# Optimization experiments

Measured on AMD Instinct MI355X. Metric: run time of the kernel, lower is better.

The kernel has to match this reference:

```python
import jax, jax.numpy as jnp
import numpy as np

B, IN_DIM, L = 8, 1, 512
D_MODEL, N_LAYERS, D_STATE, HORIZON, D_CONV, EXPAND = 512, 4, 16, 96, 4, 2
D_INNER = EXPAND * D_MODEL            # 1024
DT_RANK = (D_MODEL + 15) // 16        # ceil(d_model/16) = 32
EPS = 1e-5


def setup_inputs() -> dict:
    key = jax.random.key(0)
    ks = jax.random.split(key, 10)
    s = 0.02
    f32 = jnp.float32
    return {
        "x": jax.random.normal(ks[0], (B, IN_DIM, L), f32),
        "embed_w": jax.random.normal(ks[1], (D_MODEL, IN_DIM), f32) * s,
        "embed_b": jnp.zeros((D_MODEL,), f32),
        "norm_w": jnp.ones((N_LAYERS, D_MODEL), f32),
        "in_proj_w": jax.random.normal(ks[2], (N_LAYERS, 2 * D_INNER, D_MODEL), f32) * s,
        "conv_w": jax.random.normal(ks[3], (N_LAYERS, D_INNER, D_CONV), f32) * s,
        "conv_b": jnp.zeros((N_LAYERS, D_INNER), f32),
        "x_proj_w": jax.random.normal(ks[4], (N_LAYERS, DT_RANK + 2 * D_STATE, D_INNER), f32) * s,
        "dt_w": jax.random.normal(ks[5], (N_LAYERS, D_INNER, DT_RANK), f32) * s,
        "dt_b": jax.random.uniform(ks[6], (N_LAYERS, D_INNER), f32, -4.0, -2.0),
        "A_log": jnp.log(jnp.broadcast_to(jnp.arange(1, D_STATE + 1, dtype=f32), (N_LAYERS, D_INNER, D_STATE))),
        "D": jnp.ones((N_LAYERS, D_INNER), f32),
        "out_proj_w": jax.random.normal(ks[7], (N_LAYERS, D_MODEL, D_INNER), f32) * s,
        "head_w": jax.random.normal(ks[8], (HORIZON, D_MODEL), f32) * s,
        "head_b": jnp.zeros((HORIZON,), f32),
    }


def _rmsnorm(x, w):
    return x * jax.lax.rsqrt(jnp.mean(x * x, axis=-1, keepdims=True) + EPS) * w


def _mamba_layer(x, norm_w, in_w, conv_w, conv_b, xproj_w, dt_w, dt_b, A_log, Dp, out_w):
    res = x
    h = _rmsnorm(x, norm_w)
    xz = h @ in_w.T                       # (B, L, 2*I)
    xin, z = jnp.split(xz, 2, axis=-1)
    # causal depthwise conv1d over L (left-pad d_conv-1)
    lhs = jnp.swapaxes(xin, 1, 2)         # (B, I, L)
    rhs = conv_w[:, None, :]              # (I, 1, K)
    conv = jax.lax.conv_general_dilated(
        lhs, rhs, (1,), [(D_CONV - 1, 0)],
        dimension_numbers=("NCH", "OIH", "NCH"), feature_group_count=D_INNER)
    xin = jax.nn.silu(jnp.swapaxes(conv, 1, 2) + conv_b)   # (B, L, I)
    dbc = xin @ xproj_w.T                                   # (B, L, dt_rank+2N)
    delta = jax.nn.softplus(dbc[..., :DT_RANK] @ dt_w.T + dt_b)  # (B, L, I)
    Bc = dbc[..., DT_RANK:DT_RANK + D_STATE]                # (B, L, N)
    Cc = dbc[..., DT_RANK + D_STATE:]                       # (B, L, N)
    A = -jnp.exp(A_log)                                     # (I, N)
    dA = jnp.exp(delta[..., None] * A)                      # (B, L, I, N)
    dBx = delta[..., None] * Bc[:, :, None, :] * xin[..., None]

    def step(hst, inputs):
        a, bx = inputs
        hst = a * hst + bx
        return hst, hst

    h0 = jnp.zeros((x.shape[0], D_INNER, D_STATE), x.dtype)
    _, hs = jax.lax.scan(step, h0, (jnp.swapaxes(dA, 0, 1), jnp.swapaxes(dBx, 0, 1)))
    hs = jnp.swapaxes(hs, 0, 1)                             # (B, L, I, N)
    y = jnp.einsum("blin,bln->bli", hs, Cc) + Dp * xin
    y = y * jax.nn.silu(z)
    return res + y @ out_w.T


def reference(x, embed_w, embed_b, norm_w, in_proj_w, conv_w, conv_b, x_proj_w,
              dt_w, dt_b, A_log, D, out_proj_w, head_w, head_b):
    h = jnp.swapaxes(x, 1, 2) @ embed_w.T + embed_b         # (B, L, d_model)
    for i in range(N_LAYERS):
        h = _mamba_layer(h, norm_w[i], in_proj_w[i], conv_w[i], conv_b[i],
                         x_proj_w[i], dt_w[i], dt_b[i], A_log[i], D[i], out_proj_w[i])
    return h[:, -1, :] @ head_w.T + head_b                  # (B, horizon)
```

## Files before the change

kernel.cpp:

```cpp
#include <hip/hip_runtime.h>
#include <hip/hip_bf16.h>

#define B_  8
#define L_  512
#define DM  512
#define NL  4
#define DS  16
#define HOR 96
#define DC  4
#define DI  1024
#define DTR 32

#define CHUNK 16
#define NCHK (L_/CHUNK)

typedef __bf16 bf16_t;
typedef __bf16 b8_t __attribute__((ext_vector_type(8)));
typedef float  f4_t __attribute__((ext_vector_type(4)));

#define LOG2E 1.44269504088896f

__device__ __forceinline__ float sigmoidf_(float x){ return 1.f/(1.f+__expf(-x)); }

__device__ __forceinline__ void async16(const bf16_t* g, bf16_t* l){
  __builtin_amdgcn_global_load_lds((const __attribute__((address_space(1))) void*)g,
                                   (__attribute__((address_space(3))) void*)l, 16, 0, 0);
}

__global__ __launch_bounds__(256) void k_prep(const float* __restrict__ p0, bf16_t* __restrict__ o0,
                                              const float* __restrict__ p1, bf16_t* __restrict__ o1,
                                              const float* __restrict__ p2, bf16_t* __restrict__ o2,
                                              const float* __restrict__ p3, bf16_t* __restrict__ o3,
                                              const float* __restrict__ x, const float* __restrict__ ew,
                                              const float* __restrict__ eb, float* __restrict__ h){
  int blk = blockIdx.x;
  if (blk < 6528){
    int j = blk*256 + threadIdx.x;
    const int S0=1048576, S1=65536, S2=32768;
    const float* src; bf16_t* dst;
    if (j < S0){ src=p0; dst=o0; }
    else if ((j-=S0) < S1){ src=p1; dst=o1; }
    else if ((j-=S1) < S2){ src=p2; dst=o2; }
    else { j-=S2; src=p3; dst=o3; }
    f4_t v = ((const f4_t*)src)[j];
    bf16_t* o = dst + (size_t)j*4;
    o[0]=(bf16_t)v[0]; o[1]=(bf16_t)v[1]; o[2]=(bf16_t)v[2]; o[3]=(bf16_t)v[3];
  } else {
    int j = (blk-6528)*256 + threadIdx.x;
    int idx = j*4;
    int d = idx & (DM-1); int t = idx >> 9;
    float xv = x[t];
    f4_t w = *(const f4_t*)(ew + d);
    f4_t b = *(const f4_t*)(eb + d);
    f4_t v;
    #pragma unroll
    for (int c=0;c<4;c++) v[c] = xv*w[c] + b[c];
    *(f4_t*)(h + idx) = v;
  }
}

__global__ __launch_bounds__(256) void k_rms(const float* __restrict__ h, const float* __restrict__ w,
                                             bf16_t* __restrict__ o){
  int t = blockIdx.x; int tid = threadIdx.x;
  const float* hp = h + (size_t)t*DM;
  float v0 = hp[tid], v1 = hp[tid+256];
  float s = v0*v0 + v1*v1;
  #pragma unroll
  for (int m=32;m;m>>=1) s += __shfl_xor(s, m);
  __shared__ float red[4];
  if ((tid&63)==0) red[tid>>6]=s;
  __syncthreads();
  float tot = red[0]+red[1]+red[2]+red[3];
  float sc = rsqrtf(tot*(1.f/DM) + 1e-5f);
  o[(size_t)t*DM + tid]       = (bf16_t)(v0*sc*w[tid]);
  o[(size_t)t*DM + tid + 256] = (bf16_t)(v1*sc*w[tid+256]);
}

__global__ __launch_bounds__(256) void k_g128(const bf16_t* __restrict__ A, int lda,
                                              const bf16_t* __restrict__ W, int ldw,
                                              int K, bf16_t* __restrict__ Cbf, int ldc){
  __shared__ bf16_t As[4*128*32];
  __shared__ bf16_t Ws[4*128*32];
  int tid = threadIdx.x;
  int m0 = blockIdx.y*128, n0 = blockIdx.x*128;
  int wave = tid>>6, lane = tid&63;
  int wm = (wave>>1)*64, wn = (wave&1)*64;
  int lr = lane&15, q = lane>>4;
  int rs = tid>>2, cs = (tid&3)*8;
  f4_t acc[4][4] = {};
  for (int k0=0;k0<K;k0+=128){
    #pragma unroll
    for (int p=0;p<4;p++){
      #pragma unroll
      for (int s=0;s<2;s++){
        int row = s*64 + rs;
        async16(A + (size_t)(m0+row)*lda + k0 + p*32 + cs, As + p*4096 + s*2048 + tid*8);
        async16(W + (size_t)(n0+row)*ldw + k0 + p*32 + cs, Ws + p*4096 + s*2048 + tid*8);
      }
    }
    __syncthreads();
    #pragma unroll
    for (int p=0;p<4;p++){
      b8_t a[4], b[4];
      #pragma unroll
      for (int i=0;i<4;i++) a[i] = *(const b8_t*)(As + p*4096 + (wm+i*16+lr)*32 + q*8);
      #pragma unroll
      for (int j=0;j<4;j++) b[j] = *(const b8_t*)(Ws + p*4096 + (wn+j*16+lr)*32 + q*8);
      #pragma unroll
      for (int i=0;i<4;i++)
        #pragma unroll
        for (int j=0;j<4;j++)
          acc[i][j] = __builtin_amdgcn_mfma_f32_16x16x32_bf16(a[i], b[j], acc[i][j], 0,0,0);
    }
    __syncthreads();
  }
  #pragma unroll
  for (int i=0;i<4;i++)
  #pragma unroll
  for (int j=0;j<4;j++){
    int col = n0 + wn + j*16 + lr;
    int rb  = m0 + wm + i*16 + q*4;
    #pragma unroll
    for (int r=0;r<4;r++)
      Cbf[(size_t)(rb+r)*ldc + col] = (bf16_t)acc[i][j][r];
  }
}

__global__ __launch_bounds__(256) void k_gout64(const bf16_t* __restrict__ A,
                                                const bf16_t* __restrict__ W,
                                                float* __restrict__ C){
  __shared__ bf16_t As[8*64*32];
  __shared__ bf16_t Ws[8*64*32];
  int tid = threadIdx.x;
  int m0 = blockIdx.y*64, n0 = blockIdx.x*64;
  int wave = tid>>6, lane = tid&63;
  int wm = (wave>>1)*32, wn = (wave&1)*32;
  int lr = lane&15, q = lane>>4;
  int e0 = tid*8, r0 = e0>>5, c0 = e0&31;
  f4_t acc[2][2] = {};
  for (int k0=0;k0<DI;k0+=256){
    #pragma unroll
    for (int p=0;p<8;p++){
      async16(A + (size_t)(m0+r0)*DI + k0 + p*32 + c0, As + p*2048 + e0);
      async16(W + (size_t)(n0+r0)*DI + k0 + p*32 + c0, Ws + p*2048 + e0);
    }
    __syncthreads();
    #pragma unroll
    for (int p=0;p<8;p++){
      b8_t a[2], b[2];
      #pragma unroll
      for (int i=0;i<2;i++) a[i] = *(const b8_t*)(As + p*2048 + (wm+i*16+lr)*32 + q*8);
      #pragma unroll
      for (int j=0;j<2;j++) b[j] = *(const b8_t*)(Ws + p*2048 + (wn+j*16+lr)*32 + q*8);
      #pragma unroll
      for (int i=0;i<2;i++)
        #pragma unroll
        for (int j=0;j<2;j++)
          acc[i][j] = __builtin_amdgcn_mfma_f32_16x16x32_bf16(a[i], b[j], acc[i][j], 0,0,0);
    }
    __syncthreads();
  }
  #pragma unroll
  for (int i=0;i<2;i++)
  #pragma unroll
  for (int j=0;j<2;j++){
    int col = n0 + wn + j*16 + lr;
    int rb  = m0 + wm + i*16 + q*4;
    #pragma unroll
    for (int r=0;r<4;r++){
      size_t off = (size_t)(rb+r)*DM + col;
      C[off] = C[off] + acc[i][j][r];
    }
  }
}

__global__ __launch_bounds__(256) void k_dbc(const bf16_t* __restrict__ xzbf, const float* __restrict__ cw,
                                             const float* __restrict__ cb, const bf16_t* __restrict__ wxp,
                                             float* __restrict__ part, bf16_t* __restrict__ xinbf){
  __shared__ bf16_t As[4*64*32];
  __shared__ bf16_t Ws[4*64*32];
  int tid = threadIdx.x;
  int m0 = blockIdx.x*64;
  int z = blockIdx.y;
  int kbase = z*128;
  int wave = tid>>6, lane = tid&63;
  int wm = (wave>>1)*32, wn = (wave&1)*32;
  int lr = lane&15, q = lane>>4;
  int e0 = tid*8, r0 = e0>>5, c0 = e0&31;
  int gt = m0 + r0;
  int l  = gt & (L_-1);
  f4_t acc[2][2] = {};
  #pragma unroll
  for (int p=0;p<4;p++){
    int ch = kbase + p*32 + c0;
    float cv[8];
    #pragma unroll
    for (int c=0;c<8;c++) cv[c] = cb[ch+c];
    #pragma unroll
    for (int k=0;k<DC;k++){
      if (l + k - (DC-1) >= 0){
        b8_t xv = *(const b8_t*)(xzbf + (size_t)(gt + k - (DC-1))*(2*DI) + ch);
        #pragma unroll
        for (int c=0;c<8;c++) cv[c] += (float)xv[c] * cw[(ch+c)*DC + k];
      }
    }
    b8_t av;
    #pragma unroll
    for (int c=0;c<8;c++){ float s = cv[c]*sigmoidf_(cv[c]); av[c] = (bf16_t)s; }
    *(b8_t*)(As + p*2048 + e0) = av;
    *(b8_t*)(xinbf + (size_t)gt*DI + ch) = av;
    async16(wxp + (size_t)r0*DI + kbase + p*32 + c0, Ws + p*2048 + e0);
  }
  __syncthreads();
  #pragma unroll
  for (int p=0;p<4;p++){
    b8_t a[2], b[2];
    #pragma unroll
    for (int i=0;i<2;i++) a[i] = *(const b8_t*)(As + p*2048 + (wm+i*16+lr)*32 + q*8);
    #pragma unroll
    for (int j=0;j<2;j++) b[j] = *(const b8_t*)(Ws + p*2048 + (wn+j*16+lr)*32 + q*8);
    #pragma unroll
    for (int i=0;i<2;i++)
      #pragma unroll
      for (int j=0;j<2;j++)
        acc[i][j] = __builtin_amdgcn_mfma_f32_16x16x32_bf16(a[i], b[j], acc[i][j], 0,0,0);
  }
  float* P = part + (size_t)z*(B_*L_*64);
  #pragma unroll
  for (int i=0;i<2;i++)
  #pragma unroll
  for (int j=0;j<2;j++){
    int col = wn + j*16 + lr;
    int rb  = m0 + wm + i*16 + q*4;
    #pragma unroll
    for (int r=0;r<4;r++) P[(size_t)(rb+r)*64 + col] = acc[i][j][r];
  }
}

__global__ __launch_bounds__(256) void k_dt(const float* __restrict__ part, const bf16_t* __restrict__ wdt,
                                            const float* __restrict__ dtb, float* __restrict__ dbc,
                                            bf16_t* __restrict__ delta){
  __shared__ bf16_t As[64*32];
  __shared__ bf16_t Ws[64*32];
  int tid = threadIdx.x;
  int m0 = blockIdx.y*64, n0 = blockIdx.x*64;
  const size_t S = (size_t)B_*L_*64;
  int r0 = tid>>2, c0 = (tid&3)*8;
  int gt = m0 + r0;
  size_t base = (size_t)gt*64 + c0;
  f4_t s0 = *(const f4_t*)(part + base);
  f4_t s1 = *(const f4_t*)(part + base + 4);
  #pragma unroll
  for (int z=1;z<8;z++){
    s0 += *(const f4_t*)(part + z*S + base);
    s1 += *(const f4_t*)(part + z*S + base + 4);
  }
  b8_t av;
  #pragma unroll
  for (int c=0;c<4;c++){ av[c] = (bf16_t)s0[c]; av[4+c] = (bf16_t)s1[c]; }
  *(b8_t*)(As + tid*8) = av;
  if (n0 == 0){
    f4_t t0 = *(const f4_t*)(part + base + 32);
    f4_t t1 = *(const f4_t*)(part + base + 36);
    #pragma unroll
    for (int z=1;z<8;z++){
      t0 += *(const f4_t*)(part + z*S + base + 32);
      t1 += *(const f4_t*)(part + z*S + base + 36);
    }
    *(f4_t*)(dbc + base + 32) = t0;
    *(f4_t*)(dbc + base + 36) = t1;
  }
  async16(wdt + (size_t)(n0+r0)*DTR + c0, Ws + tid*8);
  __syncthreads();
  int wave = tid>>6, lane = tid&63;
  int wm = (wave>>1)*32, wn = (wave&1)*32;
  int lr = lane&15, q = lane>>4;
  b8_t a[2], b[2];
  #pragma unroll
  for (int i=0;i<2;i++) a[i] = *(const b8_t*)(As + (wm+i*16+lr)*32 + q*8);
  #pragma unroll
  for (int j=0;j<2;j++) b[j] = *(const b8_t*)(Ws + (wn+j*16+lr)*32 + q*8);
  f4_t acc[2][2] = {};
  #pragma unroll
  for (int i=0;i<2;i++)
    #pragma unroll
    for (int j=0;j<2;j++)
      acc[i][j] = __builtin_amdgcn_mfma_f32_16x16x32_bf16(a[i], b[j], acc[i][j], 0,0,0);
  #pragma unroll
  for (int i=0;i<2;i++)
  #pragma unroll
  for (int j=0;j<2;j++){
    int col = n0 + wn + j*16 + lr;
    int rb  = m0 + wm + i*16 + q*4;
    #pragma unroll
    for (int r=0;r<4;r++){
      float xv = acc[i][j][r] + dtb[col];
      float v = (xv>20.f)?xv:log1pf(__expf(xv));
      delta[(size_t)(rb+r)*DI + col] = (bf16_t)v;
    }
  }
}

__global__ __launch_bounds__(256) void k_scan_p1(const bf16_t* __restrict__ delta, const bf16_t* __restrict__ xin,
                                                 const float* __restrict__ dbc, const float* __restrict__ Alog,
                                                 bf16_t* __restrict__ hend, bf16_t* __restrict__ aprod){
  __shared__ bf16_t des[CHUNK][256];
  __shared__ bf16_t xs[CHUNK][256];
  __shared__ float Bs[CHUNK][DS];
  int tid = threadIdx.x;
  int blk = blockIdx.x;
  int chgrp = blk & 3;
  int chunk = (blk>>2) & (NCHK-1);
  int b = blk >> 7;
  int ch0 = chgrp<<8;
  int ch = ch0 + tid;
  int t0 = (b<<9) + chunk*CHUNK;
  #pragma unroll
  for (int idx=tid; idx<CHUNK*32; idx+=256){
    int row = idx>>5, c = (idx&31)*8;
    *(b8_t*)(&des[row][c]) = *(const b8_t*)(delta + (size_t)(t0+row)*DI + ch0 + c);
    *(b8_t*)(&xs[row][c])  = *(const b8_t*)(xin   + (size_t)(t0+row)*DI + ch0 + c);
  }
  {
    int ll = tid>>4, n = tid&15;
    Bs[ll][n] = dbc[(t0+ll)*64 + DTR + n];
  }
  __syncthreads();
  float An2[DS], h[DS];
  const f4_t* Ap = (const f4_t*)(Alog + ch*DS);
  #pragma unroll
  for (int v=0;v<4;v++){
    f4_t a4 = Ap[v];
    #pragma unroll
    for (int k=0;k<4;k++){ An2[v*4+k] = -__expf(a4[k])*LOG2E; h[v*4+k]=0.f; }
  }
  float sde = 0.f;
  #pragma unroll
  for (int l=0;l<CHUNK;l++){
    float de = (float)des[l][tid];
    float xv = (float)xs[l][tid];
    float dx = de*xv;
    sde += de;
    #pragma unroll
    for (int n=0;n<DS;n++){
      float dA = exp2f(de*An2[n]);
      h[n] = dA*h[n] + dx*Bs[l][n];
    }
  }
  size_t base = ((size_t)chunk*(B_*DI) + (b<<10) + ch)*DS;
  b8_t hv[2], av[2];
  #pragma unroll
  for (int v=0;v<2;v++)
    #pragma unroll
    for (int k=0;k<8;k++){
      hv[v][k] = (bf16_t)h[v*8+k];
      av[v][k] = (bf16_t)exp2f(An2[v*8+k]*sde);
    }
  ((b8_t*)(hend + base))[0] = hv[0]; ((b8_t*)(hend + base))[1] = hv[1];
  ((b8_t*)(aprod + base))[0] = av[0]; ((b8_t*)(aprod + base))[1] = av[1];
}

__global__ __launch_bounds__(256) void k_scan_p2(const bf16_t* __restrict__ hend, bf16_t* __restrict__ ap_hin){
  int g = blockIdx.x*256 + threadIdx.x;
  float h = 0.f;
  for (int c=0;c<NCHK;c++){
    size_t off = (size_t)c*(B_*DI*DS) + g;
    float a = (float)ap_hin[off];
    float e = (float)hend[off];
    ap_hin[off] = (bf16_t)h;
    h = a*h + e;
  }
}

__global__ __launch_bounds__(256) void k_scan_p3(const bf16_t* __restrict__ delta, const bf16_t* __restrict__ xz,
                                                 const bf16_t* __restrict__ xin,
                                                 const float* __restrict__ dbc, const float* __restrict__ Alog,
                                                 const bf16_t* __restrict__ hin, const float* __restrict__ Dp,
                                                 bf16_t* __restrict__ ybf){
  __shared__ bf16_t des[CHUNK][256];
  __shared__ bf16_t xs[CHUNK][256];
  __shared__ bf16_t zs[CHUNK][256];
  __shared__ float Bs[CHUNK][DS];
  __shared__ float Cs[CHUNK][DS];
  int tid = threadIdx.x;
  int blk = blockIdx.x;
  int chgrp = blk & 3;
  int chunk = (blk>>2) & (NCHK-1);
  int b = blk >> 7;
  int ch0 = chgrp<<8;
  int ch = ch0 + tid;
  int t0 = (b<<9) + chunk*CHUNK;
  #pragma unroll
  for (int idx=tid; idx<CHUNK*32; idx+=256){
    int row = idx>>5, c = (idx&31)*8;
    *(b8_t*)(&des[row][c]) = *(const b8_t*)(delta + (size_t)(t0+row)*DI + ch0 + c);
    *(b8_t*)(&xs[row][c])  = *(const b8_t*)(xin   + (size_t)(t0+row)*DI + ch0 + c);
    *(b8_t*)(&zs[row][c])  = *(const b8_t*)(xz + (size_t)(t0+row)*(2*DI) + DI + ch0 + c);
  }
  {
    int ll = tid>>4, n = tid&15;
    Bs[ll][n] = dbc[(t0+ll)*64 + DTR + n];
    Cs[ll][n] = dbc[(t0+ll)*64 + DTR + DS + n];
  }
  __syncthreads();
  float An2[DS], h[DS];
  const f4_t* Ap = (const f4_t*)(Alog + ch*DS);
  size_t base = ((size_t)chunk*(B_*DI) + (b<<10) + ch)*DS;
  b8_t h0 = ((const b8_t*)(hin + base))[0];
  b8_t h1 = ((const b8_t*)(hin + base))[1];
  #pragma unroll
  for (int v=0;v<4;v++){
    f4_t a4 = Ap[v];
    #pragma unroll
    for (int k=0;k<4;k++){
      An2[v*4+k] = -__expf(a4[k])*LOG2E;
      int idx = v*4+k;
      h[idx] = (idx<8) ? (float)h0[idx] : (float)h1[idx-8];
    }
  }
  float Dv = Dp[ch];
  bf16_t* yp = ybf + (size_t)t0*DI + ch;
  #pragma unroll
  for (int l=0;l<CHUNK;l++){
    float de = (float)des[l][tid];
    float zv = (float)zs[l][tid];
    float xv = (float)xs[l][tid];
    float dx = de*xv;
    float y = 0.f;
    #pragma unroll
    for (int n=0;n<DS;n++){
      float dA = exp2f(de*An2[n]);
      h[n] = dA*h[n] + dx*Bs[l][n];
      y += h[n]*Cs[l][n];
    }
    y = (y + Dv*xv) * (zv * sigmoidf_(zv));
    yp[(size_t)l*DI] = (bf16_t)y;
  }
}

__global__ __launch_bounds__(256) void k_head(const float* __restrict__ h, const float* __restrict__ hw,
                                              const float* __restrict__ hb, float* __restrict__ out){
  int wave = threadIdx.x>>6, lane = threadIdx.x&63;
  int gw = blockIdx.x*4 + wave;
  int b = gw / HOR, hh = gw % HOR;
  const float* hp = h + ((size_t)b*L_ + (L_-1))*DM;
  const float* wp = hw + (size_t)hh*DM;
  float s = 0.f;
  #pragma unroll
  for (int k=0;k<DM;k+=64) s += hp[k+lane]*wp[k+lane];
  #pragma unroll
  for (int m=32;m;m>>=1) s += __shfl_xor(s, m);
  if (lane==0) out[gw] = s + hb[hh];
}

extern "C" void kernel_launch(void* const* d_in, const int* in_sizes, int n_in,
                              void* d_out, int out_size, void* d_ws, size_t ws_size,
                              hipStream_t stream){
  const float* x    = (const float*)d_in[0];
  const float* ew   = (const float*)d_in[1];
  const float* eb   = (const float*)d_in[2];
  const float* nw   = (const float*)d_in[3];
  const float* ipw  = (const float*)d_in[4];
  const float* cw   = (const float*)d_in[5];
  const float* cb   = (const float*)d_in[6];
  const float* xpw  = (const float*)d_in[7];
  const float* dtw  = (const float*)d_in[8];
  const float* dtb  = (const float*)d_in[9];
  const float* alog = (const float*)d_in[10];
  const float* Dp   = (const float*)d_in[11];
  const float* opw  = (const float*)d_in[12];
  const float* hw   = (const float*)d_in[13];
  const float* hb   = (const float*)d_in[14];
  float* out = (float*)d_out;

  char* ws = (char*)d_ws;
  size_t o = 0;
  float*  h      = (float*)(ws + o);  o += (size_t)8<<20;
  bf16_t* hnorm  = (bf16_t*)(ws + o); o += (size_t)4<<20;
  bf16_t* xzbf   = (bf16_t*)(ws + o); o += (size_t)16<<20;
  bf16_t* xinbf  = (bf16_t*)(ws + o); o += (size_t)8<<20;
  bf16_t* delta  = (bf16_t*)(ws + o); o += (size_t)8<<20;
  bf16_t* ybf    = (bf16_t*)(ws + o); o += (size_t)8<<20;
  float*  dbc    = (float*)(ws + o);  o += (size_t)1<<20;
  float*  dbcp   = (float*)(ws + o);  o += (size_t)8<<20;
  bf16_t* w_in   = (bf16_t*)(ws + o); o += (size_t)8<<20;
  bf16_t* w_out  = (bf16_t*)(ws + o); o += (size_t)4<<20;
  bf16_t* w_xp   = (bf16_t*)(ws + o); o += (size_t)1<<19;
  bf16_t* w_dt   = (bf16_t*)(ws + o); o += (size_t)1<<18;
  bf16_t* hend   = (bf16_t*)(ws + o); o += (size_t)8<<20;
  bf16_t* aphin  = (bf16_t*)(ws + o); o += (size_t)8<<20;

  k_prep<<<8576,256,0,stream>>>(ipw, w_in, xpw, w_xp, dtw, w_dt, opw, w_out,
                                x, ew, eb, h);

  for (int i=0;i<NL;i++){
    k_rms<<<B_*L_,256,0,stream>>>(h, nw + i*DM, hnorm);
    k_g128<<<dim3(2*DI/128, B_*L_/128),256,0,stream>>>(
        hnorm, DM, w_in + (size_t)i*2*DI*DM, DM, DM, xzbf, 2*DI);
    k_dbc<<<dim3(B_*L_/64, 8),256,0,stream>>>(xzbf, cw + i*DI*DC, cb + i*DI,
                                              w_xp + (size_t)i*64*DI, dbcp, xinbf);
    k_dt<<<dim3(DI/64, B_*L_/64),256,0,stream>>>(dbcp, w_dt + (size_t)i*DI*DTR,
                                                 dtb + i*DI, dbc, delta);
    k_scan_p1<<<B_*NCHK*4,256,0,stream>>>(delta, xinbf, dbc, alog + i*DI*DS, hend, aphin);
    k_scan_p2<<<(B_*DI*DS)/256,256,0,stream>>>(hend, aphin);
    k_scan_p3<<<B_*NCHK*4,256,0,stream>>>(delta, xzbf, xinbf, dbc, alog + i*DI*DS,
                                          aphin, Dp + i*DI, ybf);
    k_gout64<<<dim3(DM/64, B_*L_/64),256,0,stream>>>(ybf, w_out + (size_t)i*DM*DI, h);
  }
  k_head<<<(B_*HOR)/4,256,0,stream>>>(h, hw, hb, out);
}
```

Before: 609.4 us.

## Fuse RMSNorm into in-proj GEMM epilogue via folded weights and row sum-of-squares

Removes the per-layer RMSNorm kernel. The norm weight is folded into the bf16 in_proj weights during prep, and the out-projection epilogue writes a bf16 copy of the residual plus per-row sum-of-squares through atomics. The in_proj GEMM then applies the rsqrt scale per row in its epilogue. The out-proj GEMM is also restructured so each wave takes a split-K slice of a 64x64 tile, with the partial sums reduced through swizzled LDS. This saves one kernel launch and a full activation read/write per layer, at the cost of atomic float sums (nondeterministic order) and an extra LDS reduction.

```diff
diff --git a/kernel.cpp b/kernel.cpp
--- a/kernel.cpp
+++ b/kernel.cpp
@@ -16,6 +16,7 @@
 
 typedef __bf16 bf16_t;
 typedef __bf16 b8_t __attribute__((ext_vector_type(8)));
+typedef __bf16 b4_t __attribute__((ext_vector_type(4)));
 typedef float  f4_t __attribute__((ext_vector_type(4)));
 
 #define LOG2E 1.44269504088896f
@@ -32,21 +33,30 @@
                                               const float* __restrict__ p2, bf16_t* __restrict__ o2,
                                               const float* __restrict__ p3, bf16_t* __restrict__ o3,
                                               const float* __restrict__ x, const float* __restrict__ ew,
-                                              const float* __restrict__ eb, float* __restrict__ h){
+                                              const float* __restrict__ eb, float* __restrict__ h,
+                                              const float* __restrict__ nw, bf16_t* __restrict__ hbf,
+                                              float* __restrict__ sumsq){
   int blk = blockIdx.x;
   if (blk < 6528){
     int j = blk*256 + threadIdx.x;
     const int S0=1048576, S1=65536, S2=32768;
     const float* src; bf16_t* dst;
-    if (j < S0){ src=p0; dst=o0; }
+    const float* fold = nullptr;
+    if (j < S0){
+      src=p0; dst=o0;
+      int idx4 = j<<2;
+      fold = nw + ((idx4>>20)*DM) + (idx4 & (DM-1));
+    }
     else if ((j-=S0) < S1){ src=p1; dst=o1; }
     else if ((j-=S1) < S2){ src=p2; dst=o2; }
     else { j-=S2; src=p3; dst=o3; }
     f4_t v = ((const f4_t*)src)[j];
+    if (fold){ f4_t f = *(const f4_t*)fold; v *= f; }
     bf16_t* o = dst + (size_t)j*4;
     o[0]=(bf16_t)v[0]; o[1]=(bf16_t)v[1]; o[2]=(bf16_t)v[2]; o[3]=(bf16_t)v[3];
   } else {
-    int j = (blk-6528)*256 + threadIdx.x;
+    int tid = threadIdx.x;
+    int j = (blk-6528)*256 + tid;
     int idx = j*4;
     int d = idx & (DM-1); int t = idx >> 9;
     float xv = x[t];
@@ -56,29 +66,26 @@
     #pragma unroll
     for (int c=0;c<4;c++) v[c] = xv*w[c] + b[c];
     *(f4_t*)(h + idx) = v;
-  }
-}
-
-__global__ __launch_bounds__(256) void k_rms(const float* __restrict__ h, const float* __restrict__ w,
-                                             bf16_t* __restrict__ o){
-  int t = blockIdx.x; int tid = threadIdx.x;
-  const float* hp = h + (size_t)t*DM;
-  float v0 = hp[tid], v1 = hp[tid+256];
-  float s = v0*v0 + v1*v1;
-  #pragma unroll
-  for (int m=32;m;m>>=1) s += __shfl_xor(s, m);
-  __shared__ float red[4];
-  if ((tid&63)==0) red[tid>>6]=s;
-  __syncthreads();
-  float tot = red[0]+red[1]+red[2]+red[3];
-  float sc = rsqrtf(tot*(1.f/DM) + 1e-5f);
-  o[(size_t)t*DM + tid]       = (bf16_t)(v0*sc*w[tid]);
-  o[(size_t)t*DM + tid + 256] = (bf16_t)(v1*sc*w[tid+256]);
+    b4_t hv;
+    #pragma unroll
+    for (int c=0;c<4;c++) hv[c] = (bf16_t)v[c];
+    *(b4_t*)(hbf + idx) = hv;
+    float s = v[0]*v[0]+v[1]*v[1]+v[2]*v[2]+v[3]*v[3];
+    #pragma unroll
+    for (int m=32;m;m>>=1) s += __shfl_xor(s, m);
+    __shared__ float red2[4];
+    if ((tid&63)==0) red2[tid>>6] = s;
+    __syncthreads();
+    int tb = (blk-6528)*2;
+    if (tid==0)   sumsq[tb]   = red2[0]+red2[1];
+    if (tid==128) sumsq[tb+1] = red2[2]+red2[3];
+  }
 }
 
 __global__ __launch_bounds__(256) void k_g128(const bf16_t* __restrict__ A, int lda,
                                               const bf16_t* __restrict__ W, int ldw,
-                                              int K, bf16_t* __restrict__ Cbf, int ldc){
+                                              int K, bf16_t* __restrict__ Cbf, int ldc,
+                                              const float* __restrict__ sumsq){
   __shared__ bf16_t As[4*128*32];
   __shared__ bf16_t Ws[4*128*32];
   int tid = threadIdx.x;
@@ -115,29 +122,36 @@
     __syncthreads();
   }
   #pragma unroll
-  for (int i=0;i<4;i++)
-  #pragma unroll
-  for (int j=0;j<4;j++){
-    int col = n0 + wn + j*16 + lr;
-    int rb  = m0 + wm + i*16 + q*4;
-    #pragma unroll
-    for (int r=0;r<4;r++)
-      Cbf[(size_t)(rb+r)*ldc + col] = (bf16_t)acc[i][j][r];
-  }
-}
-
-__global__ __launch_bounds__(256) void k_gout64(const bf16_t* __restrict__ A,
-                                                const bf16_t* __restrict__ W,
-                                                float* __restrict__ C){
-  __shared__ bf16_t As[8*64*32];
-  __shared__ bf16_t Ws[8*64*32];
+  for (int i=0;i<4;i++){
+    int rb = m0 + wm + i*16 + q*4;
+    f4_t sc;
+    #pragma unroll
+    for (int r=0;r<4;r++) sc[r] = rsqrtf(sumsq[rb+r]*(1.f/DM) + 1e-5f);
+    #pragma unroll
+    for (int j=0;j<4;j++){
+      int col = n0 + wn + j*16 + lr;
+      #pragma unroll
+      for (int r=0;r<4;r++)
+        Cbf[(size_t)(rb+r)*ldc + col] = (bf16_t)(acc[i][j][r]*sc[r]);
+    }
+  }
+}
+
+__global__ __launch_bounds__(256) void k_gout(const bf16_t* __restrict__ A,
+                                              const bf16_t* __restrict__ W,
+                                              float* __restrict__ C,
+                                              bf16_t* __restrict__ hbf,
+                                              float* __restrict__ sumsq){
+  __shared__ __align__(16) char sm[65536];
+  bf16_t* As = (bf16_t*)sm;
+  bf16_t* Ws = (bf16_t*)(sm + 32768);
+  float*  red = (float*)sm;
   int tid = threadIdx.x;
   int m0 = blockIdx.y*64, n0 = blockIdx.x*64;
   int wave = tid>>6, lane = tid&63;
-  int wm = (wave>>1)*32, wn = (wave&1)*32;
   int lr = lane&15, q = lane>>4;
   int e0 = tid*8, r0 = e0>>5, c0 = e0&31;
-  f4_t acc[2][2] = {};
+  f4_t acc[4][4] = {};
   for (int k0=0;k0<DI;k0+=256){
     #pragma unroll
     for (int p=0;p<8;p++){
@@ -146,31 +160,55 @@
     }
     __syncthreads();
     #pragma unroll
-    for (int p=0;p<8;p++){
-      b8_t a[2], b[2];
-      #pragma unroll
-      for (int i=0;i<2;i++) a[i] = *(const b8_t*)(As + p*2048 + (wm+i*16+lr)*32 + q*8);
-      #pragma unroll
-      for (int j=0;j<2;j++) b[j] = *(const b8_t*)(Ws + p*2048 + (wn+j*16+lr)*32 + q*8);
-      #pragma unroll
-      for (int i=0;i<2;i++)
+    for (int s=0;s<2;s++){
+      const bf16_t* Ap = As + (2*wave+s)*2048;
+      const bf16_t* Wp = Ws + (2*wave+s)*2048;
+      b8_t a[4], b[4];
+      #pragma unroll
+      for (int i=0;i<4;i++) a[i] = *(const b8_t*)(Ap + (i*16+lr)*32 + q*8);
+      #pragma unroll
+      for (int j=0;j<4;j++) b[j] = *(const b8_t*)(Wp + (j*16+lr)*32 + q*8);
+      #pragma unroll
+      for (int i=0;i<4;i++)
         #pragma unroll
-        for (int j=0;j<2;j++)
+        for (int j=0;j<4;j++)
           acc[i][j] = __builtin_amdgcn_mfma_f32_16x16x32_bf16(a[i], b[j], acc[i][j], 0,0,0);
     }
     __syncthreads();
   }
   #pragma unroll
-  for (int i=0;i<2;i++)
-  #pragma unroll
-  for (int j=0;j<2;j++){
-    int col = n0 + wn + j*16 + lr;
-    int rb  = m0 + wm + i*16 + q*4;
-    #pragma unroll
-    for (int r=0;r<4;r++){
-      size_t off = (size_t)(rb+r)*DM + col;
-      C[off] = C[off] + acc[i][j][r];
-    }
+  for (int i=0;i<4;i++)
+  #pragma unroll
+  for (int j=0;j<4;j++)
+  #pragma unroll
+  for (int r=0;r<4;r++){
+    int rl = i*16 + q*4 + r;
+    int t4 = ((rl ^ (rl>>2)) & 3) << 2;
+    int c4 = j*4 + (lr>>2);
+    red[wave*4096 + rl*64 + ((c4 ^ t4)<<2) + (lr&3)] = acc[i][j][r];
+  }
+  __syncthreads();
+  #pragma unroll
+  for (int g=0;g<4;g++){
+    int row = g*16 + (tid>>4);
+    int t4 = ((row ^ (row>>2)) & 3) << 2;
+    int fo = row*64 + (((tid&15) ^ t4) << 2);
+    f4_t v = *(const f4_t*)(red + fo);
+    v += *(const f4_t*)(red + 4096 + fo);
+    v += *(const f4_t*)(red + 8192 + fo);
+    v += *(const f4_t*)(red + 12288 + fo);
+    size_t off = (size_t)(m0+row)*DM + n0 + (tid&15)*4;
+    f4_t c = *(const f4_t*)(C + off);
+    c += v;
+    *(f4_t*)(C + off) = c;
+    b4_t hv;
+    #pragma unroll
+    for (int k=0;k<4;k++) hv[k] = (bf16_t)c[k];
+    *(b4_t*)(hbf + off) = hv;
+    float s2 = c[0]*c[0]+c[1]*c[1]+c[2]*c[2]+c[3]*c[3];
+    s2 += __shfl_xor(s2,1); s2 += __shfl_xor(s2,2);
+    s2 += __shfl_xor(s2,4); s2 += __shfl_xor(s2,8);
+    if ((tid&15)==0) atomicAdd(sumsq + m0 + row, s2);
   }
 }
 
@@ -360,7 +398,9 @@
   ((b8_t*)(aprod + base))[0] = av[0]; ((b8_t*)(aprod + base))[1] = av[1];
 }
 
-__global__ __launch_bounds__(256) void k_scan_p2(const bf16_t* __restrict__ hend, bf16_t* __restrict__ ap_hin){
+__global__ __launch_bounds__(256) void k_scan_p2(const bf16_t* __restrict__ hend, bf16_t* __restrict__ ap_hin,
+                                                 float* __restrict__ sumsq){
+  if (blockIdx.x < 16) sumsq[(blockIdx.x<<8) | threadIdx.x] = 0.f;
   int g = blockIdx.x*256 + threadIdx.x;
   float h = 0.f;
   for (int c=0;c<NCHK;c++){
@@ -476,7 +516,7 @@
   char* ws = (char*)d_ws;
   size_t o = 0;
   float*  h      = (float*)(ws + o);  o += (size_t)8<<20;
-  bf16_t* hnorm  = (bf16_t*)(ws + o); o += (size_t)4<<20;
+  bf16_t* hbf    = (bf16_t*)(ws + o); o += (size_t)4<<20;
   bf16_t* xzbf   = (bf16_t*)(ws + o); o += (size_t)16<<20;
   bf16_t* xinbf  = (bf16_t*)(ws + o); o += (size_t)8<<20;
   bf16_t* delta  = (bf16_t*)(ws + o); o += (size_t)8<<20;
@@ -489,23 +529,23 @@
   bf16_t* w_dt   = (bf16_t*)(ws + o); o += (size_t)1<<18;
   bf16_t* hend   = (bf16_t*)(ws + o); o += (size_t)8<<20;
   bf16_t* aphin  = (bf16_t*)(ws + o); o += (size_t)8<<20;
+  float*  sumsq  = (float*)(ws + o);  o += (size_t)1<<16;
 
   k_prep<<<8576,256,0,stream>>>(ipw, w_in, xpw, w_xp, dtw, w_dt, opw, w_out,
-                                x, ew, eb, h);
+                                x, ew, eb, h, nw, hbf, sumsq);
 
   for (int i=0;i<NL;i++){
-    k_rms<<<B_*L_,256,0,stream>>>(h, nw + i*DM, hnorm);
     k_g128<<<dim3(2*DI/128, B_*L_/128),256,0,stream>>>(
-        hnorm, DM, w_in + (size_t)i*2*DI*DM, DM, DM, xzbf, 2*DI);
+        hbf, DM, w_in + (size_t)i*2*DI*DM, DM, DM, xzbf, 2*DI, sumsq);
     k_dbc<<<dim3(B_*L_/64, 8),256,0,stream>>>(xzbf, cw + i*DI*DC, cb + i*DI,
                                               w_xp + (size_t)i*64*DI, dbcp, xinbf);
     k_dt<<<dim3(DI/64, B_*L_/64),256,0,stream>>>(dbcp, w_dt + (size_t)i*DI*DTR,
                                                  dtb + i*DI, dbc, delta);
     k_scan_p1<<<B_*NCHK*4,256,0,stream>>>(delta, xinbf, dbc, alog + i*DI*DS, hend, aphin);
-    k_scan_p2<<<(B_*DI*DS)/256,256,0,stream>>>(hend, aphin);
+    k_scan_p2<<<(B_*DI*DS)/256,256,0,stream>>>(hend, aphin, sumsq);
     k_scan_p3<<<B_*NCHK*4,256,0,stream>>>(delta, xzbf, xinbf, dbc, alog + i*DI*DS,
                                           aphin, Dp + i*DI, ybf);
-    k_gout64<<<dim3(DM/64, B_*L_/64),256,0,stream>>>(ybf, w_out + (size_t)i*DM*DI, h);
+    k_gout<<<dim3(DM/64, B_*L_/64),256,0,stream>>>(ybf, w_out + (size_t)i*DM*DI, h, hbf, sumsq);
   }
   k_head<<<(B_*HOR)/4,256,0,stream>>>(h, hw, hb, out);
 }
```

After: 602.2 us. No clear change (-1.2%).
